# Optimization experiments

Measured on AMD Instinct MI355X. Metric: run time of the kernel, lower is better.

## Reference

```python
import jax, jax.numpy as jnp
import numpy as np

N_NODES = 100000
N_EDGES = 3200000
F_IN = 16
HID = 64
K = 4
N_LAYERS = 3
SLOPE = 0.01  # LeakyReLU default negative slope


def _gcn_norm(src, dst, edge_weight, n):
    # PyG gcn_norm with add_self_loops=False: deg over targets
    deg = jax.ops.segment_sum(edge_weight, dst, num_segments=n)
    dinv = jnp.where(deg > 0, jax.lax.rsqrt(jnp.maximum(deg, 1e-30)), 0.0)
    return dinv[src] * edge_weight * dinv[dst]


def _tag_conv(x, src, dst, norm, Ws, b):
    # out = sum_{k=0..K} (A_norm^k x) @ Ws[k] + b ; Ws: [K+1, in, out]
    out = x @ Ws[0]
    h = x
    for k in range(1, Ws.shape[0]):
        msg = norm[:, None] * h[src]                      # [E, in]
        h = jax.ops.segment_sum(msg, dst, num_segments=x.shape[0])
        out = out + h @ Ws[k]
    return out + b


def leaky_relu(x):
    return jnp.where(x >= 0, x, SLOPE * x)


def setup_inputs() -> dict:
    key = jax.random.key(0)
    ks = jax.random.split(key, 10)
    x = jax.random.normal(ks[0], (N_NODES, F_IN), dtype=jnp.float32)
    edge_index = jax.random.randint(ks[1], (2, N_EDGES), 0, N_NODES, dtype=jnp.int64)
    edge_weight = jax.random.uniform(ks[2], (N_EDGES,), dtype=jnp.float32)
    batch = jnp.zeros((N_NODES,), dtype=jnp.int64)
    s1 = 1.0 / np.sqrt(F_IN)
    s2 = 1.0 / np.sqrt(HID)
    W1 = jax.random.uniform(ks[3], (K + 1, F_IN, HID), jnp.float32, -s1, s1)
    b1 = jnp.zeros((HID,), jnp.float32)
    W2 = jax.random.uniform(ks[4], (N_LAYERS - 1, K + 1, HID, HID), jnp.float32, -s2, s2)
    b2 = jnp.zeros((N_LAYERS - 1, HID), jnp.float32)
    Wout = jax.random.uniform(ks[5], (HID, 1), jnp.float32, -s2, s2)
    bout = jnp.zeros((1,), jnp.float32)
    return {"x": x, "edge_index": edge_index, "edge_weight": edge_weight,
            "batch": batch, "W1": W1, "b1": b1, "W2": W2, "b2": b2,
            "Wout": Wout, "bout": bout}


def reference(x, edge_index, edge_weight, batch, W1, b1, W2, b2, Wout, bout):
    src, dst = edge_index[0], edge_index[1]
    norm = _gcn_norm(src, dst, edge_weight, x.shape[0])
    h = _tag_conv(x, src, dst, norm, W1, b1)
    h = leaky_relu(h)  # dropout p=0 -> identity (inference)
    for i in range(N_LAYERS - 1):
        h = _tag_conv(h, src, dst, norm, W2[i], b2[i])
        h = leaky_relu(h)
    # reghead_layers == 1 -> singleLinear
    return h @ Wout + bout
```

## Files before the change

kernel.cpp:

```cpp
#include <hip/hip_runtime.h>
#include <hip/hip_cooperative_groups.h>

namespace cg = cooperative_groups;


typedef unsigned long long u64;
typedef unsigned int u32;

__device__ __forceinline__ float h2f(unsigned short u) {
  _Float16 h;
  __builtin_memcpy(&h, &u, 2);
  return (float)h;
}
__device__ __forceinline__ unsigned short f2h(float f) {
  _Float16 h = (_Float16)f;
  unsigned short u;
  __builtin_memcpy(&u, &h, 2);
  return u;
}
__device__ __forceinline__ ushort4 pack_h(float4 v) {
  ushort4 r;
  r.x = f2h(v.x); r.y = f2h(v.y); r.z = f2h(v.z); r.w = f2h(v.w);
  return r;
}
__device__ __forceinline__ float4 unpack_h(ushort4 u) {
  return make_float4(h2f(u.x), h2f(u.y), h2f(u.z), h2f(u.w));
}
__device__ __forceinline__ void dec_ep(u32 u, int& s, float& w) {
  s = (int)(u & 0x1FFFFu);
  w = h2f((unsigned short)(u >> 17));
}


__global__ __launch_bounds__(256) void k_hist(const int* __restrict__ dst, u32* __restrict__ H,
                                              int E, int CH, int NB,
                                              const float4* __restrict__ x4,
                                              ushort4* __restrict__ xh, int n4) {
  __shared__ u32 hc[1024];
  int tid = threadIdx.x, blk = blockIdx.x, nblk = gridDim.x;
  for (int i = tid; i < 1024; i += 256) hc[i] = 0;
  for (int i = blk * 256 + tid; i < n4; i += nblk * 256) xh[i] = pack_h(x4[i]);
  __syncthreads();
  int e0 = blk * CH, e1 = min(E, e0 + CH);
  for (int e = e0 + tid; e < e1; e += 256) atomicAdd(&hc[((u32)dst[e]) >> 7], 1u);
  __syncthreads();
  for (int c = tid; c < NB; c += 256) H[(size_t)c * nblk + blk] = hc[c];
}

__global__ void scanH_blocks(u32* __restrict__ H, u32* __restrict__ bsum, int n) {
  __shared__ u32 s[256];
  int tid = threadIdx.x;
  int i = blockIdx.x * 256 + tid;
  u32 v = (i < n) ? H[i] : 0;
  s[tid] = v;
  __syncthreads();
#pragma unroll
  for (int off = 1; off < 256; off <<= 1) {
    u32 t = (tid >= off) ? s[tid - off] : 0;
    __syncthreads();
    s[tid] += t;
    __syncthreads();
  }
  if (i < n) H[i] = s[tid] - v;
  if (tid == 255) bsum[blockIdx.x] = s[255];
}

__global__ void scanH_sums(u32* __restrict__ bsum, int nb) {
  __shared__ u32 s[1024];
  int tid = threadIdx.x;
  u32 v = (tid < nb) ? bsum[tid] : 0;
  s[tid] = v;
  __syncthreads();
#pragma unroll
  for (int off = 1; off < 1024; off <<= 1) {
    u32 t = (tid >= off) ? s[tid - off] : 0;
    __syncthreads();
    s[tid] += t;
    __syncthreads();
  }
  if (tid < nb) bsum[tid] = s[tid] - v;
}

__global__ void scanH_add(u32* __restrict__ H, const u32* __restrict__ bsum, int n) {
  int i = blockIdx.x * blockDim.x + threadIdx.x;
  if (i < n) H[i] += bsum[i >> 8];
}

__global__ __launch_bounds__(256) void k_scatter(const int* __restrict__ src,
                                                 const int* __restrict__ dst,
                                                 const float* __restrict__ w,
                                                 const u32* __restrict__ H,
                                                 u64* __restrict__ sorted, int E, int CH, int NB) {
  __shared__ u32 cur[1024];
  int tid = threadIdx.x, blk = blockIdx.x, nblk = gridDim.x;
  for (int c = tid; c < NB; c += 256) cur[c] = H[(size_t)c * nblk + blk];
  __syncthreads();
  int e0 = blk * CH, e1 = min(E, e0 + CH);
  for (int e = e0 + tid; e < e1; e += 256) {
    int d = dst[e];
    int c = ((u32)d) >> 7;
    u32 p = atomicAdd(&cur[c], 1u);
    u64 it = (u64)(u32)src[e] | ((u64)((u32)d & 127u) << 17) |
             ((u64)__float_as_uint(w[e]) << 24);
    sorted[p] = it;
  }
}

#define BCAP 6144
__global__ __launch_bounds__(256) void k_bucket(u64* __restrict__ sorted,
                                                const u32* __restrict__ H, int NBLK,
                                                int* __restrict__ ptr, float* __restrict__ dinv,
                                                int N, int E, int NB) {
  __shared__ u64 stage[BCAP];
  __shared__ u32 cnt[128], base[128], cur[128], tmp[128];
  __shared__ float ws[128];
  int c = blockIdx.x, tid = threadIdx.x;
  int b0 = (int)H[(size_t)c * NBLK];
  int b1 = (c + 1 < NB) ? (int)H[(size_t)(c + 1) * NBLK] : E;
  int m = b1 - b0;
  if (tid < 128) { cnt[tid] = 0; ws[tid] = 0.f; }
  __syncthreads();
  for (int i = tid; i < m; i += 256) {
    u64 it = sorted[b0 + i];
    stage[i] = it;
    int lo = (int)((it >> 17) & 127u);
    atomicAdd(&cnt[lo], 1u);
    atomicAdd(&ws[lo], __uint_as_float((u32)(it >> 24)));
  }
  __syncthreads();
  u32 v = (tid < 128) ? cnt[tid] : 0;
  if (tid < 128) tmp[tid] = v;
  __syncthreads();
#pragma unroll
  for (int off = 1; off < 128; off <<= 1) {
    u32 t = 0;
    if (tid < 128 && tid >= off) t = tmp[tid - off];
    __syncthreads();
    if (tid < 128) tmp[tid] += t;
    __syncthreads();
  }
  if (tid < 128) {
    base[tid] = tmp[tid] - v;
    cur[tid] = tmp[tid] - v;
    int node = c * 128 + tid;
    if (node < N) {
      ptr[node] = b0 + (int)base[tid];
      float d = ws[tid];
      dinv[node] = (d > 0.f) ? rsqrtf(fmaxf(d, 1e-30f)) : 0.f;
    }
  }
  if (c == NB - 1 && tid == 0) ptr[N] = E;
  __syncthreads();
  for (int i = tid; i < m; i += 256) {
    u64 it = stage[i];
    int lo = (int)((it >> 17) & 127u);
    u32 p = atomicAdd(&cur[lo], 1u);
    sorted[b0 + (int)p] = it;
  }
}

__global__ __launch_bounds__(256) void k_pack(const u64* __restrict__ sorted,
                                              const float* __restrict__ dinv,
                                              const u32* __restrict__ H, int NBLK,
                                              u32* __restrict__ ep, int E, int NB) {
  int c = blockIdx.x;
  int b0 = (int)H[(size_t)c * NBLK];
  int b1 = (c + 1 < NB) ? (int)H[(size_t)(c + 1) * NBLK] : E;
  for (int i = b0 + threadIdx.x; i < b1; i += 256) {
    u64 it = sorted[i];
    int s = (int)(it & 0x1FFFFu);
    int dn = c * 128 + (int)((it >> 17) & 127u);
    float wv = __uint_as_float((u32)(it >> 24));
    float nv = dinv[s] * wv * dinv[dn];
    ep[i] = ((u32)f2h(nv) << 17) | (u32)s;
  }
}

__device__ __forceinline__ void acc_e(float4& a, u32 pe, ushort4 h) {
  float w = h2f((unsigned short)(pe >> 17));
  a.x = fmaf(w, h2f(h.x), a.x); a.y = fmaf(w, h2f(h.y), a.y);
  a.z = fmaf(w, h2f(h.z), a.z); a.w = fmaf(w, h2f(h.w), a.w);
}

template <int F4>
__device__ __forceinline__ float4 gather(const int* __restrict__ ptr, const u32* __restrict__ ep,
                                         const ushort4* __restrict__ hin, int node, int f4) {
  int e0 = ptr[node], e1 = ptr[node + 1];
  float4 a = make_float4(0.f, 0.f, 0.f, 0.f);
  int e = e0;
  while (e < e1 && (e & 3)) {
    u32 pe = ep[e];
    acc_e(a, pe, hin[(u32)(pe & 0x1FFFFu) * F4 + f4]);
    ++e;
  }
  int nq = (e1 - e) >> 2;
  if (nq > 0) {
    uint4 p = *(const uint4*)(ep + e);
    ushort4 h0 = hin[(u32)(p.x & 0x1FFFFu) * F4 + f4];
    ushort4 h1 = hin[(u32)(p.y & 0x1FFFFu) * F4 + f4];
    ushort4 h2 = hin[(u32)(p.z & 0x1FFFFu) * F4 + f4];
    ushort4 h3 = hin[(u32)(p.w & 0x1FFFFu) * F4 + f4];
    for (int q = 1; q < nq; ++q) {
      uint4 pn = *(const uint4*)(ep + e + 4 * q);
      ushort4 g0 = hin[(u32)(pn.x & 0x1FFFFu) * F4 + f4];
      ushort4 g1 = hin[(u32)(pn.y & 0x1FFFFu) * F4 + f4];
      ushort4 g2 = hin[(u32)(pn.z & 0x1FFFFu) * F4 + f4];
      ushort4 g3 = hin[(u32)(pn.w & 0x1FFFFu) * F4 + f4];
      acc_e(a, p.x, h0); acc_e(a, p.y, h1);
      acc_e(a, p.z, h2); acc_e(a, p.w, h3);
      p = pn; h0 = g0; h1 = g1; h2 = g2; h3 = g3;
    }
    acc_e(a, p.x, h0); acc_e(a, p.y, h1);
    acc_e(a, p.z, h2); acc_e(a, p.w, h3);
    e += nq * 4;
  }
  while (e < e1) {
    u32 pe = ep[e];
    acc_e(a, pe, hin[(u32)(pe & 0x1FFFFu) * F4 + f4]);
    ++e;
  }
  return a;
}

__device__ __forceinline__ void acc8(float4& a0, float4& a1, u32 pe, uint4 r) {
  float w = h2f((unsigned short)(pe >> 17));
  a0.x = fmaf(w, h2f((unsigned short)(r.x & 0xFFFFu)), a0.x);
  a0.y = fmaf(w, h2f((unsigned short)(r.x >> 16)), a0.y);
  a0.z = fmaf(w, h2f((unsigned short)(r.y & 0xFFFFu)), a0.z);
  a0.w = fmaf(w, h2f((unsigned short)(r.y >> 16)), a0.w);
  a1.x = fmaf(w, h2f((unsigned short)(r.z & 0xFFFFu)), a1.x);
  a1.y = fmaf(w, h2f((unsigned short)(r.z >> 16)), a1.y);
  a1.z = fmaf(w, h2f((unsigned short)(r.w & 0xFFFFu)), a1.z);
  a1.w = fmaf(w, h2f((unsigned short)(r.w >> 16)), a1.w);
}

__device__ __forceinline__ void gather64o(const int* __restrict__ ptr, const u32* __restrict__ ep,
                                          const ushort4* __restrict__ hin, int node,
                                          int f8, int o, float4& a0, float4& a1) {
  int e0 = ptr[node], e1 = ptr[node + 1];
  const u32 foff = 2u * (u32)f8;
  int e = e0;
  while (e < e1 && (e & 3)) {
    if ((e & 1) == o) {
      u32 pe = ep[e];
      uint4 r = *(const uint4*)(hin + ((u32)(pe & 0x1FFFFu) * 16u + foff));
      acc8(a0, a1, pe, r);
    }
    ++e;
  }
  int nq = (e1 - e) >> 2;
  int q = o;
  if (q < nq) {
    uint4 p = *(const uint4*)(ep + e + 4 * q);
    uint4 r0 = *(const uint4*)(hin + ((u32)(p.x & 0x1FFFFu) * 16u + foff));
    uint4 r1 = *(const uint4*)(hin + ((u32)(p.y & 0x1FFFFu) * 16u + foff));
    for (;;) {
      uint4 r2 = *(const uint4*)(hin + ((u32)(p.z & 0x1FFFFu) * 16u + foff));
      uint4 r3 = *(const uint4*)(hin + ((u32)(p.w & 0x1FFFFu) * 16u + foff));
      acc8(a0, a1, p.x, r0);
      acc8(a0, a1, p.y, r1);
      int qn = q + 2;
      if (qn >= nq) {
        acc8(a0, a1, p.z, r2);
        acc8(a0, a1, p.w, r3);
        break;
      }
      uint4 pn = *(const uint4*)(ep + e + 4 * qn);
      r0 = *(const uint4*)(hin + ((u32)(pn.x & 0x1FFFFu) * 16u + foff));
      r1 = *(const uint4*)(hin + ((u32)(pn.y & 0x1FFFFu) * 16u + foff));
      acc8(a0, a1, p.z, r2);
      acc8(a0, a1, p.w, r3);
      p = pn; q = qn;
    }
  }
  e += nq * 4;
  while (e < e1) {
    if ((e & 1) == o) {
      u32 pe = ep[e];
      uint4 r = *(const uint4*)(hin + ((u32)(pe & 0x1FFFFu) * 16u + foff));
      acc8(a0, a1, pe, r);
    }
    ++e;
  }
}

__device__ __forceinline__ void mm_acc(const float* __restrict__ tl, const float4* __restrict__ Wl,
                                       int ln, int j4, float4& a) {
#pragma unroll 8
  for (int i = 0; i < 64; ++i) {
    float tv = tl[ln * 64 + ((((i >> 2) ^ ln) << 2) | (i & 3))];
    float4 wv = Wl[i * 16 + j4];
    a.x = fmaf(tv, wv.x, a.x); a.y = fmaf(tv, wv.y, a.y);
    a.z = fmaf(tv, wv.z, a.z); a.w = fmaf(tv, wv.w, a.w);
  }
}

template <int NC>
__global__ __launch_bounds__(256) void mega_k(
    const int* __restrict__ ptr, const u32* __restrict__ ep,
    ushort4* __restrict__ hb0, ushort4* __restrict__ hb1, ushort4* __restrict__ hb2,
    const float* __restrict__ W2, const float* __restrict__ b2,
    const float* __restrict__ Wout, const float* __restrict__ bout,
    float* __restrict__ outv, int n) {
  cg::grid_group grid = cg::this_grid();
  __shared__ float4 Wl[1024];
  __shared__ float4 tl4[256];
  const float* tl = (const float*)tl4;
  const int tid = threadIdx.x, j4 = tid & 15, ln = tid >> 4;
  const int nb = (int)gridDim.x;
  float4 acc[NC];

  for (int L = 0; L < 2; ++L) {
    const float* WL = W2 + (size_t)L * 5 * 4096;
#pragma unroll
    for (int c = 0; c < NC; ++c) acc[c] = make_float4(0.f, 0.f, 0.f, 0.f);

    {
      const float4* W04 = (const float4*)WL;
      for (int i = tid; i < 1024; i += 256) Wl[i] = W04[i];
      __syncthreads();
#pragma unroll
      for (int c = 0; c < NC; ++c) {
        int node = (c * nb + (int)blockIdx.x) * 16 + ln;
        float4 own = make_float4(0.f, 0.f, 0.f, 0.f);
        if (node < n) own = unpack_h(hb2[(size_t)node * 16 + j4]);
        tl4[ln * 16 + (j4 ^ ln)] = own;
        mm_acc(tl, Wl, ln, j4, acc[c]);
      }
      __syncthreads();
    }

    for (int k = 1; k <= 4; ++k) {
      const ushort4* gsrc = (k == 1) ? hb2 : ((k == 3) ? hb1 : hb0);
      ushort4* gdst = (k == 2) ? hb1 : hb0;
      const bool last = (k == 4);
      const float4* Wk4 = (const float4*)(WL + (size_t)k * 4096);
      for (int i = tid; i < 1024; i += 256) Wl[i] = Wk4[i];
      __syncthreads();
#pragma unroll
      for (int c = 0; c < NC; ++c) {
        int node = (c * nb + (int)blockIdx.x) * 16 + ln;
        float4 t = make_float4(0.f, 0.f, 0.f, 0.f);
        if (node < n) {
          t = gather<16>(ptr, ep, gsrc, node, j4);
          if (!last) gdst[(size_t)node * 16 + j4] = pack_h(t);
        }
        tl4[ln * 16 + (j4 ^ ln)] = t;
        mm_acc(tl, Wl, ln, j4, acc[c]);
      }
      if (last) {
        const float4* bias4 = (const float4*)(b2 + (size_t)L * 64);
#pragma unroll
        for (int c = 0; c < NC; ++c) {
          int node = (c * nb + (int)blockIdx.x) * 16 + ln;
          if (node >= n) continue;
          float4 a = acc[c];
          float4 b = bias4[j4];
          a.x += b.x; a.y += b.y; a.z += b.z; a.w += b.w;
          a.x = (a.x >= 0.f) ? a.x : 0.01f * a.x;
          a.y = (a.y >= 0.f) ? a.y : 0.01f * a.y;
          a.z = (a.z >= 0.f) ? a.z : 0.01f * a.z;
          a.w = (a.w >= 0.f) ? a.w : 0.01f * a.w;
          if (L == 0) {
            hb2[(size_t)node * 16 + j4] = pack_h(a);
          } else {
            float v = a.x * Wout[4 * j4] + a.y * Wout[4 * j4 + 1] +
                      a.z * Wout[4 * j4 + 2] + a.w * Wout[4 * j4 + 3];
            v += __shfl_down(v, 8, 16);
            v += __shfl_down(v, 4, 16);
            v += __shfl_down(v, 2, 16);
            v += __shfl_down(v, 1, 16);
            if (j4 == 0) outv[node] = v + bout[0];
          }
        }
      }
      if (!(L == 1 && k == 4)) {
        __threadfence();
        grid.sync();
      }
    }
  }
}

template <bool FIRST, bool LAST, bool HEAD>
__launch_bounds__(256)
__global__ void ptag64_k(const int* __restrict__ ptr, const u32* __restrict__ ep,
                         const ushort4* __restrict__ hin, ushort4* __restrict__ hout,
                         const float4* __restrict__ Wk4, const float4* __restrict__ W04,
                         ushort4* __restrict__ acch, const float4* __restrict__ bias4,
                         const float* __restrict__ Wout, const float* __restrict__ bout,
                         float* __restrict__ outv, int n) {
  __shared__ float4 Wl[1024];
  __shared__ float4 tl4[256];
  const float* tl = (const float*)tl4;
  int tid = threadIdx.x;
  for (int i = tid; i < 1024; i += 256) Wl[i] = Wk4[i];
  int gid = blockIdx.x * 256 + tid;
  int node = gid >> 4, j4 = gid & 15, ln = tid >> 4;
  const int o = j4 >> 3, f8 = j4 & 7;

  float4 a0 = make_float4(0.f, 0.f, 0.f, 0.f);
  float4 a1 = make_float4(0.f, 0.f, 0.f, 0.f);
  if (node < n) gather64o(ptr, ep, hin, node, f8, o, a0, a1);
  a0.x += __shfl_xor(a0.x, 8, 16); a0.y += __shfl_xor(a0.y, 8, 16);
  a0.z += __shfl_xor(a0.z, 8, 16); a0.w += __shfl_xor(a0.w, 8, 16);
  a1.x += __shfl_xor(a1.x, 8, 16); a1.y += __shfl_xor(a1.y, 8, 16);
  a1.z += __shfl_xor(a1.z, 8, 16); a1.w += __shfl_xor(a1.w, 8, 16);
  float4 t = (o == 0) ? a0 : a1;
  int g = 2 * f8 + o;
  if (node < n && !LAST) hout[(size_t)node * 16 + g] = pack_h(t);
  tl4[ln * 16 + (g ^ ln)] = t;
  __syncthreads();

  float4 a = make_float4(0.f, 0.f, 0.f, 0.f);
  if (!FIRST && node < n) a = unpack_h(acch[(size_t)node * 16 + j4]);
  mm_acc(tl, Wl, ln, j4, a);
  if (FIRST) {
    __syncthreads();
    for (int i = tid; i < 1024; i += 256) Wl[i] = W04[i];
    float4 own = make_float4(0.f, 0.f, 0.f, 0.f);
    if (node < n) own = unpack_h(hin[(size_t)node * 16 + j4]);
    tl4[ln * 16 + (j4 ^ ln)] = own;
    __syncthreads();
    mm_acc(tl, Wl, ln, j4, a);
  }
  if (node >= n) return;

  if (LAST) {
    float4 b = bias4[j4];
    a.x += b.x; a.y += b.y; a.z += b.z; a.w += b.w;
    a.x = (a.x >= 0.f) ? a.x : 0.01f * a.x;
    a.y = (a.y >= 0.f) ? a.y : 0.01f * a.y;
    a.z = (a.z >= 0.f) ? a.z : 0.01f * a.z;
    a.w = (a.w >= 0.f) ? a.w : 0.01f * a.w;
    if (HEAD) {
      float v = a.x * Wout[4 * j4] + a.y * Wout[4 * j4 + 1] +
                a.z * Wout[4 * j4 + 2] + a.w * Wout[4 * j4 + 3];
      v += __shfl_down(v, 8, 16);
      v += __shfl_down(v, 4, 16);
      v += __shfl_down(v, 2, 16);
      v += __shfl_down(v, 1, 16);
      if (j4 == 0) outv[node] = v + bout[0];
    } else {
      hout[(size_t)node * 16 + j4] = pack_h(a);
    }
  } else {
    acch[(size_t)node * 16 + j4] = pack_h(a);
  }
}

template <bool FIRST, bool LAST>
__launch_bounds__(256)
__global__ void ptag16_k(const int* __restrict__ ptr, const u32* __restrict__ ep,
                         const ushort4* __restrict__ hin, ushort4* __restrict__ hout,
                         const float4* __restrict__ Wk4, const float4* __restrict__ W04,
                         ushort4* __restrict__ acch, const float4* __restrict__ bias4,
                         ushort4* __restrict__ outbuf, int n) {
  __shared__ float4 Wl[256];
  __shared__ float4 W0l[FIRST ? 256 : 1];
  __shared__ float4 tl4[64 * 5];
  const float* tl = (const float*)tl4;
  int tid = threadIdx.x;
  Wl[tid] = Wk4[tid];
  if (FIRST) W0l[tid] = W04[tid];
  int gid = blockIdx.x * 256 + tid;
  int node = gid >> 2, q = tid & 3, ln = tid >> 2;

  float4 t = make_float4(0.f, 0.f, 0.f, 0.f);
  if (node < n) {
    t = gather<4>(ptr, ep, hin, node, q);
    if (!LAST) hout[(size_t)node * 4 + q] = pack_h(t);
  }
  tl4[ln * 5 + q] = t;
  __syncthreads();

  float4 a[4];
#pragma unroll
  for (int c = 0; c < 4; ++c) a[c] = make_float4(0.f, 0.f, 0.f, 0.f);
  if (!FIRST && node < n) {
#pragma unroll
    for (int c = 0; c < 4; ++c) a[c] = unpack_h(acch[(size_t)node * 16 + 4 * q + c]);
  }
#pragma unroll 4
  for (int i = 0; i < 16; ++i) {
    float tv = tl[ln * 20 + i];
#pragma unroll
    for (int c = 0; c < 4; ++c) {
      float4 wv = Wl[i * 16 + 4 * q + c];
      a[c].x = fmaf(tv, wv.x, a[c].x); a[c].y = fmaf(tv, wv.y, a[c].y);
      a[c].z = fmaf(tv, wv.z, a[c].z); a[c].w = fmaf(tv, wv.w, a[c].w);
    }
  }
  if (FIRST) {
    __syncthreads();
    float4 own = make_float4(0.f, 0.f, 0.f, 0.f);
    if (node < n) own = unpack_h(hin[(size_t)node * 4 + q]);
    tl4[ln * 5 + q] = own;
    __syncthreads();
#pragma unroll 4
    for (int i = 0; i < 16; ++i) {
      float tv = tl[ln * 20 + i];
#pragma unroll
      for (int c = 0; c < 4; ++c) {
        float4 wv = W0l[i * 16 + 4 * q + c];
        a[c].x = fmaf(tv, wv.x, a[c].x); a[c].y = fmaf(tv, wv.y, a[c].y);
        a[c].z = fmaf(tv, wv.z, a[c].z); a[c].w = fmaf(tv, wv.w, a[c].w);
      }
    }
  }
  if (node >= n) return;

  if (LAST) {
#pragma unroll
    for (int c = 0; c < 4; ++c) {
      float4 b = bias4[4 * q + c];
      a[c].x += b.x; a[c].y += b.y; a[c].z += b.z; a[c].w += b.w;
      a[c].x = (a[c].x >= 0.f) ? a[c].x : 0.01f * a[c].x;
      a[c].y = (a[c].y >= 0.f) ? a[c].y : 0.01f * a[c].y;
      a[c].z = (a[c].z >= 0.f) ? a[c].z : 0.01f * a[c].z;
      a[c].w = (a[c].w >= 0.f) ? a[c].w : 0.01f * a[c].w;
      outbuf[(size_t)node * 16 + 4 * q + c] = pack_h(a[c]);
    }
  } else {
#pragma unroll
    for (int c = 0; c < 4; ++c) acch[(size_t)node * 16 + 4 * q + c] = pack_h(a[c]);
  }
}

extern "C" void kernel_launch(void* const* d_in, const int* in_sizes, int n_in,
                              void* d_out, int out_size, void* d_ws, size_t ws_size,
                              hipStream_t stream) {
  const float* x    = (const float*)d_in[0];
  const int*   ei   = (const int*)d_in[1];
  const float* ew   = (const float*)d_in[2];
  const float* W1   = (const float*)d_in[4];
  const float* b1   = (const float*)d_in[5];
  const float* W2   = (const float*)d_in[6];
  const float* b2   = (const float*)d_in[7];
  const float* Wout = (const float*)d_in[8];
  const float* bout = (const float*)d_in[9];
  float* out = (float*)d_out;

  const int N = in_sizes[0] / 16;
  const int E = in_sizes[2];
  const int* src = ei;
  const int* dst = ei + E;

  const int NBLK = 256;
  const int CH = (E + NBLK - 1) / NBLK;
  const int NB = (N + 127) >> 7;
  const int HN = NB * NBLK;

  char* ws = (char*)d_ws;
  size_t off = 0;
  auto alloc = [&](size_t bytes) {
    char* p = ws + off;
    off = (off + bytes + 255) & ~(size_t)255;
    return p;
  };
  u32*     H      = (u32*)alloc((size_t)HN * 4);
  u32*     bsum   = (u32*)alloc(4096);
  float*   dinv   = (float*)alloc((size_t)N * 4);
  int*     ptr    = (int*)alloc(((size_t)N + 1) * 4);
  u64*     sorted = (u64*)alloc((size_t)E * 8);
  u32*     ep     = (u32*)alloc((size_t)E * 4);
  ushort4* xh     = (ushort4*)alloc((size_t)N * 16 * 2);
  ushort4* hb0    = (ushort4*)alloc((size_t)N * 64 * 2);
  ushort4* hb1    = (ushort4*)alloc((size_t)N * 64 * 2);
  ushort4* hb2    = (ushort4*)alloc((size_t)N * 64 * 2);
  ushort4* acch   = (ushort4*)alloc((size_t)N * 64 * 2);

  k_hist<<<NBLK, 256, 0, stream>>>(dst, H, E, CH, NB, (const float4*)x, xh, N * 4);
  scanH_blocks<<<HN / 256, 256, 0, stream>>>(H, bsum, HN);
  scanH_sums<<<1, 1024, 0, stream>>>(bsum, HN / 256);
  scanH_add<<<HN / 256, 256, 0, stream>>>(H, bsum, HN);
  k_scatter<<<NBLK, 256, 0, stream>>>(src, dst, ew, H, sorted, E, CH, NB);
  k_bucket<<<NB, 256, 0, stream>>>(sorted, H, NBLK, ptr, dinv, N, E, NB);
  k_pack<<<NB, 256, 0, stream>>>(sorted, dinv, H, NBLK, ep, E, NB);

  int g4  = (N * 4 + 255) / 256;
  int g16 = (N * 16 + 255) / 256;

  auto W1k = [&](int k) { return (const float4*)(W1 + (size_t)k * 1024); };
  auto W2k = [&](int l, int k) { return (const float4*)(W2 + ((size_t)l * 5 + k) * 4096); };

  ptag16_k<true,  false><<<g4, 256, 0, stream>>>(ptr, ep, xh,  hb0, W1k(1), W1k(0), acch, nullptr, nullptr, N);
  ptag16_k<false, false><<<g4, 256, 0, stream>>>(ptr, ep, hb0, hb1, W1k(2), nullptr, acch, nullptr, nullptr, N);
  ptag16_k<false, false><<<g4, 256, 0, stream>>>(ptr, ep, hb1, hb0, W1k(3), nullptr, acch, nullptr, nullptr, N);
  ptag16_k<false, true ><<<g4, 256, 0, stream>>>(ptr, ep, hb0, nullptr, W1k(4), nullptr, acch,
                                                 (const float4*)b1, hb2, N);

  int maxB4 = 0, maxB5 = 0, maxB7 = 0;
  (void)hipOccupancyMaxActiveBlocksPerMultiprocessor(&maxB4, mega_k<4>, 256, 0);
  (void)hipOccupancyMaxActiveBlocksPerMultiprocessor(&maxB5, mega_k<5>, 256, 0);
  (void)hipOccupancyMaxActiveBlocksPerMultiprocessor(&maxB7, mega_k<7>, 256, 0);
  void* fn = nullptr;
  int grid = 0;
  if ((long)maxB4 * 256 * 16 * 4 >= (long)N) {
    fn = (void*)mega_k<4>; grid = maxB4 * 256;
  } else if ((long)maxB5 * 256 * 16 * 5 >= (long)N) {
    fn = (void*)mega_k<5>; grid = maxB5 * 256;
  } else if ((long)maxB7 * 256 * 16 * 7 >= (long)N) {
    fn = (void*)mega_k<7>; grid = maxB7 * 256;
  }

  if (fn) {
    const int* ptrA = ptr; const u32* epA = ep;
    ushort4 *h0A = hb0, *h1A = hb1, *h2A = hb2;
    const float *W2A = W2, *b2A = b2, *WoA = Wout, *boA = bout;
    float* outA = out; int nA = N;
    void* args[] = {&ptrA, &epA, &h0A, &h1A, &h2A, &W2A, &b2A, &WoA, &boA, &outA, &nA};
    hipLaunchCooperativeKernel(fn, dim3(grid), dim3(256), args, 0, stream);
  } else {
    ptag64_k<true,  false, false><<<g16, 256, 0, stream>>>(ptr, ep, hb2, hb0, W2k(0,1), W2k(0,0), acch,
                                                           nullptr, nullptr, nullptr, nullptr, N);
    ptag64_k<false, false, false><<<g16, 256, 0, stream>>>(ptr, ep, hb0, hb1, W2k(0,2), nullptr, acch,
                                                           nullptr, nullptr, nullptr, nullptr, N);
    ptag64_k<false, false, false><<<g16, 256, 0, stream>>>(ptr, ep, hb1, hb0, W2k(0,3), nullptr, acch,
                                                           nullptr, nullptr, nullptr, nullptr, N);
    ptag64_k<false, true,  false><<<g16, 256, 0, stream>>>(ptr, ep, hb0, hb2, W2k(0,4), nullptr, acch,
                                                           (const float4*)b2, nullptr, nullptr, nullptr, N);
    ptag64_k<true,  false, false><<<g16, 256, 0, stream>>>(ptr, ep, hb2, hb0, W2k(1,1), W2k(1,0), acch,
                                                           nullptr, nullptr, nullptr, nullptr, N);
    ptag64_k<false, false, false><<<g16, 256, 0, stream>>>(ptr, ep, hb0, hb1, W2k(1,2), nullptr, acch,
                                                           nullptr, nullptr, nullptr, nullptr, N);
    ptag64_k<false, false, false><<<g16, 256, 0, stream>>>(ptr, ep, hb1, hb0, W2k(1,3), nullptr, acch,
                                                           nullptr, nullptr, nullptr, nullptr, N);
    ptag64_k<false, true,  true ><<<g16, 256, 0, stream>>>(ptr, ep, hb0, nullptr, W2k(1,4), nullptr, acch,
                                                           (const float4*)(b2 + 64), Wout, bout, out, N);
  }
}
```

Baseline: 953.6 us.

## Drop cooperative mega-kernel; process four nodes per thread group in per-hop kernels

Removes the cooperative grid-synchronised mega kernel and always runs the per-hop 64-wide TAG kernels. Each 16-lane group now handles NC=4 nodes, so every weight element loaded from shared memory is reused across four node rows, and each weight tile is staged once per 64 nodes rather than once per 16. The intent is to cut grid.sync overhead and shared-memory weight traffic in exchange for more kernel launches, a larger LDS footprint (20KB+16KB) and more registers, which may lower occupancy for the latency-bound gather.

```diff
diff --git a/kernel.cpp b/kernel.cpp
--- a/kernel.cpp
+++ b/kernel.cpp
@@ -296,6 +296,22 @@
 }
 
 template <int NC>
+__device__ __forceinline__ void mm_acc_nc(const float* __restrict__ tl, const float4* __restrict__ Wl,
+                                          int ln, int j4, float4* acc) {
+#pragma unroll 8
+  for (int i = 0; i < 64; ++i) {
+    float4 wv = Wl[i * 16 + j4];
+    int sw = ln * 64 + ((((i >> 2) ^ ln) << 2) | (i & 3));
+#pragma unroll
+    for (int c = 0; c < NC; ++c) {
+      float tv = tl[c * 1024 + sw];
+      acc[c].x = fmaf(tv, wv.x, acc[c].x); acc[c].y = fmaf(tv, wv.y, acc[c].y);
+      acc[c].z = fmaf(tv, wv.z, acc[c].z); acc[c].w = fmaf(tv, wv.w, acc[c].w);
+    }
+  }
+}
+
+template <int NC>
 __global__ __launch_bounds__(256) void mega_k(
     const int* __restrict__ ptr, const u32* __restrict__ ep,
     ushort4* __restrict__ hb0, ushort4* __restrict__ hb1, ushort4* __restrict__ hb2,
@@ -314,7 +330,6 @@
     const float* WL = W2 + (size_t)L * 5 * 4096;
 #pragma unroll
     for (int c = 0; c < NC; ++c) acc[c] = make_float4(0.f, 0.f, 0.f, 0.f);
-
     {
       const float4* W04 = (const float4*)WL;
       for (int i = tid; i < 1024; i += 256) Wl[i] = W04[i];
@@ -329,7 +344,6 @@
       }
       __syncthreads();
     }
-
     for (int k = 1; k <= 4; ++k) {
       const ushort4* gsrc = (k == 1) ? hb2 : ((k == 3) ? hb1 : hb0);
       ushort4* gdst = (k == 2) ? hb1 : hb0;
@@ -382,70 +396,91 @@
   }
 }
 
-template <bool FIRST, bool LAST, bool HEAD>
+template <int NC, bool FIRST, bool LAST, bool HEAD>
 __launch_bounds__(256)
-__global__ void ptag64_k(const int* __restrict__ ptr, const u32* __restrict__ ep,
-                         const ushort4* __restrict__ hin, ushort4* __restrict__ hout,
-                         const float4* __restrict__ Wk4, const float4* __restrict__ W04,
-                         ushort4* __restrict__ acch, const float4* __restrict__ bias4,
-                         const float* __restrict__ Wout, const float* __restrict__ bout,
-                         float* __restrict__ outv, int n) {
+__global__ void ptag64nc_k(const int* __restrict__ ptr, const u32* __restrict__ ep,
+                           const ushort4* __restrict__ hin, ushort4* __restrict__ hout,
+                           const float4* __restrict__ Wk4, const float4* __restrict__ W04,
+                           ushort4* __restrict__ acch, const float4* __restrict__ bias4,
+                           const float* __restrict__ Wout, const float* __restrict__ bout,
+                           float* __restrict__ outv, int n) {
   __shared__ float4 Wl[1024];
-  __shared__ float4 tl4[256];
+  __shared__ float4 tl4[NC * 256];
   const float* tl = (const float*)tl4;
   int tid = threadIdx.x;
   for (int i = tid; i < 1024; i += 256) Wl[i] = Wk4[i];
-  int gid = blockIdx.x * 256 + tid;
-  int node = gid >> 4, j4 = gid & 15, ln = tid >> 4;
+  const int j4 = tid & 15, ln = tid >> 4;
   const int o = j4 >> 3, f8 = j4 & 7;
-
-  float4 a0 = make_float4(0.f, 0.f, 0.f, 0.f);
-  float4 a1 = make_float4(0.f, 0.f, 0.f, 0.f);
-  if (node < n) gather64o(ptr, ep, hin, node, f8, o, a0, a1);
-  a0.x += __shfl_xor(a0.x, 8, 16); a0.y += __shfl_xor(a0.y, 8, 16);
-  a0.z += __shfl_xor(a0.z, 8, 16); a0.w += __shfl_xor(a0.w, 8, 16);
-  a1.x += __shfl_xor(a1.x, 8, 16); a1.y += __shfl_xor(a1.y, 8, 16);
-  a1.z += __shfl_xor(a1.z, 8, 16); a1.w += __shfl_xor(a1.w, 8, 16);
-  float4 t = (o == 0) ? a0 : a1;
-  int g = 2 * f8 + o;
-  if (node < n && !LAST) hout[(size_t)node * 16 + g] = pack_h(t);
-  tl4[ln * 16 + (g ^ ln)] = t;
-  __syncthreads();
-
-  float4 a = make_float4(0.f, 0.f, 0.f, 0.f);
-  if (!FIRST && node < n) a = unpack_h(acch[(size_t)node * 16 + j4]);
-  mm_acc(tl, Wl, ln, j4, a);
+  const int nbase = (blockIdx.x * 16 + ln) * NC;
+
+#pragma unroll
+  for (int c = 0; c < NC; ++c) {
+    int node = nbase + c;
+    float4 a0 = make_float4(0.f, 0.f, 0.f, 0.f);
+    float4 a1 = make_float4(0.f, 0.f, 0.f, 0.f);
+    if (node < n) gather64o(ptr, ep, hin, node, f8, o, a0, a1);
+    a0.x += __shfl_xor(a0.x, 8, 16); a0.y += __shfl_xor(a0.y, 8, 16);
+    a0.z += __shfl_xor(a0.z, 8, 16); a0.w += __shfl_xor(a0.w, 8, 16);
+    a1.x += __shfl_xor(a1.x, 8, 16); a1.y += __shfl_xor(a1.y, 8, 16);
+    a1.z += __shfl_xor(a1.z, 8, 16); a1.w += __shfl_xor(a1.w, 8, 16);
+    float4 t = (o == 0) ? a0 : a1;
+    int g = 2 * f8 + o;
+    if (node < n && !LAST) hout[(size_t)node * 16 + g] = pack_h(t);
+    tl4[c * 256 + ln * 16 + (g ^ ln)] = t;
+  }
+  __syncthreads();
+
+  float4 acc[NC];
+#pragma unroll
+  for (int c = 0; c < NC; ++c) {
+    acc[c] = make_float4(0.f, 0.f, 0.f, 0.f);
+    if (!FIRST) {
+      int node = nbase + c;
+      if (node < n) acc[c] = unpack_h(acch[(size_t)node * 16 + j4]);
+    }
+  }
+  mm_acc_nc<NC>(tl, Wl, ln, j4, acc);
+
   if (FIRST) {
     __syncthreads();
     for (int i = tid; i < 1024; i += 256) Wl[i] = W04[i];
-    float4 own = make_float4(0.f, 0.f, 0.f, 0.f);
-    if (node < n) own = unpack_h(hin[(size_t)node * 16 + j4]);
-    tl4[ln * 16 + (j4 ^ ln)] = own;
-    __syncthreads();
-    mm_acc(tl, Wl, ln, j4, a);
-  }
-  if (node >= n) return;
-
-  if (LAST) {
-    float4 b = bias4[j4];
-    a.x += b.x; a.y += b.y; a.z += b.z; a.w += b.w;
-    a.x = (a.x >= 0.f) ? a.x : 0.01f * a.x;
-    a.y = (a.y >= 0.f) ? a.y : 0.01f * a.y;
-    a.z = (a.z >= 0.f) ? a.z : 0.01f * a.z;
-    a.w = (a.w >= 0.f) ? a.w : 0.01f * a.w;
-    if (HEAD) {
-      float v = a.x * Wout[4 * j4] + a.y * Wout[4 * j4 + 1] +
-                a.z * Wout[4 * j4 + 2] + a.w * Wout[4 * j4 + 3];
-      v += __shfl_down(v, 8, 16);
-      v += __shfl_down(v, 4, 16);
-      v += __shfl_down(v, 2, 16);
-      v += __shfl_down(v, 1, 16);
-      if (j4 == 0) outv[node] = v + bout[0];
+#pragma unroll
+    for (int c = 0; c < NC; ++c) {
+      int node = nbase + c;
+      float4 own = make_float4(0.f, 0.f, 0.f, 0.f);
+      if (node < n) own = unpack_h(hin[(size_t)node * 16 + j4]);
+      tl4[c * 256 + ln * 16 + (j4 ^ ln)] = own;
+    }
+    __syncthreads();
+    mm_acc_nc<NC>(tl, Wl, ln, j4, acc);
+  }
+
+#pragma unroll
+  for (int c = 0; c < NC; ++c) {
+    int node = nbase + c;
+    if (node >= n) continue;
+    float4 a = acc[c];
+    if (LAST) {
+      float4 b = bias4[j4];
+      a.x += b.x; a.y += b.y; a.z += b.z; a.w += b.w;
+      a.x = (a.x >= 0.f) ? a.x : 0.01f * a.x;
+      a.y = (a.y >= 0.f) ? a.y : 0.01f * a.y;
+      a.z = (a.z >= 0.f) ? a.z : 0.01f * a.z;
+      a.w = (a.w >= 0.f) ? a.w : 0.01f * a.w;
+      if (HEAD) {
+        float v = a.x * Wout[4 * j4] + a.y * Wout[4 * j4 + 1] +
+                  a.z * Wout[4 * j4 + 2] + a.w * Wout[4 * j4 + 3];
+        v += __shfl_down(v, 8, 16);
+        v += __shfl_down(v, 4, 16);
+        v += __shfl_down(v, 2, 16);
+        v += __shfl_down(v, 1, 16);
+        if (j4 == 0) outv[node] = v + bout[0];
+      } else {
+        hout[(size_t)node * 16 + j4] = pack_h(a);
+      }
     } else {
-      hout[(size_t)node * 16 + j4] = pack_h(a);
-    }
-  } else {
-    acch[(size_t)node * 16 + j4] = pack_h(a);
+      acch[(size_t)node * 16 + j4] = pack_h(a);
+    }
   }
 }
 
@@ -578,8 +613,9 @@
   k_bucket<<<NB, 256, 0, stream>>>(sorted, H, NBLK, ptr, dinv, N, E, NB);
   k_pack<<<NB, 256, 0, stream>>>(sorted, dinv, H, NBLK, ep, E, NB);
 
-  int g4  = (N * 4 + 255) / 256;
-  int g16 = (N * 16 + 255) / 256;
+  int g4 = (N * 4 + 255) / 256;
+  constexpr int NCP = 4;
+  int g64 = (N + 16 * NCP - 1) / (16 * NCP);
 
   auto W1k = [&](int k) { return (const float4*)(W1 + (size_t)k * 1024); };
   auto W2k = [&](int l, int k) { return (const float4*)(W2 + ((size_t)l * 5 + k) * 4096); };
@@ -590,43 +626,20 @@
   ptag16_k<false, true ><<<g4, 256, 0, stream>>>(ptr, ep, hb0, nullptr, W1k(4), nullptr, acch,
                                                  (const float4*)b1, hb2, N);
 
-  int maxB4 = 0, maxB5 = 0, maxB7 = 0;
-  (void)hipOccupancyMaxActiveBlocksPerMultiprocessor(&maxB4, mega_k<4>, 256, 0);
-  (void)hipOccupancyMaxActiveBlocksPerMultiprocessor(&maxB5, mega_k<5>, 256, 0);
-  (void)hipOccupancyMaxActiveBlocksPerMultiprocessor(&maxB7, mega_k<7>, 256, 0);
-  void* fn = nullptr;
-  int grid = 0;
-  if ((long)maxB4 * 256 * 16 * 4 >= (long)N) {
-    fn = (void*)mega_k<4>; grid = maxB4 * 256;
-  } else if ((long)maxB5 * 256 * 16 * 5 >= (long)N) {
-    fn = (void*)mega_k<5>; grid = maxB5 * 256;
-  } else if ((long)maxB7 * 256 * 16 * 7 >= (long)N) {
-    fn = (void*)mega_k<7>; grid = maxB7 * 256;
-  }
-
-  if (fn) {
-    const int* ptrA = ptr; const u32* epA = ep;
-    ushort4 *h0A = hb0, *h1A = hb1, *h2A = hb2;
-    const float *W2A = W2, *b2A = b2, *WoA = Wout, *boA = bout;
-    float* outA = out; int nA = N;
-    void* args[] = {&ptrA, &epA, &h0A, &h1A, &h2A, &W2A, &b2A, &WoA, &boA, &outA, &nA};
-    hipLaunchCooperativeKernel(fn, dim3(grid), dim3(256), args, 0, stream);
-  } else {
-    ptag64_k<true,  false, false><<<g16, 256, 0, stream>>>(ptr, ep, hb2, hb0, W2k(0,1), W2k(0,0), acch,
-                                                           nullptr, nullptr, nullptr, nullptr, N);
-    ptag64_k<false, false, false><<<g16, 256, 0, stream>>>(ptr, ep, hb0, hb1, W2k(0,2), nullptr, acch,
-                                                           nullptr, nullptr, nullptr, nullptr, N);
-    ptag64_k<false, false, false><<<g16, 256, 0, stream>>>(ptr, ep, hb1, hb0, W2k(0,3), nullptr, acch,
-                                                           nullptr, nullptr, nullptr, nullptr, N);
-    ptag64_k<false, true,  false><<<g16, 256, 0, stream>>>(ptr, ep, hb0, hb2, W2k(0,4), nullptr, acch,
-                                                           (const float4*)b2, nullptr, nullptr, nullptr, N);
-    ptag64_k<true,  false, false><<<g16, 256, 0, stream>>>(ptr, ep, hb2, hb0, W2k(1,1), W2k(1,0), acch,
-                                                           nullptr, nullptr, nullptr, nullptr, N);
-    ptag64_k<false, false, false><<<g16, 256, 0, stream>>>(ptr, ep, hb0, hb1, W2k(1,2), nullptr, acch,
-                                                           nullptr, nullptr, nullptr, nullptr, N);
-    ptag64_k<false, false, false><<<g16, 256, 0, stream>>>(ptr, ep, hb1, hb0, W2k(1,3), nullptr, acch,
-                                                           nullptr, nullptr, nullptr, nullptr, N);
-    ptag64_k<false, true,  true ><<<g16, 256, 0, stream>>>(ptr, ep, hb0, nullptr, W2k(1,4), nullptr, acch,
-                                                           (const float4*)(b2 + 64), Wout, bout, out, N);
-  }
-}
+  ptag64nc_k<NCP, true,  false, false><<<g64, 256, 0, stream>>>(ptr, ep, hb2, hb0, W2k(0,1), W2k(0,0), acch,
+                                                                nullptr, nullptr, nullptr, nullptr, N);
+  ptag64nc_k<NCP, false, false, false><<<g64, 256, 0, stream>>>(ptr, ep, hb0, hb1, W2k(0,2), nullptr, acch,
+                                                                nullptr, nullptr, nullptr, nullptr, N);
+  ptag64nc_k<NCP, false, false, false><<<g64, 256, 0, stream>>>(ptr, ep, hb1, hb0, W2k(0,3), nullptr, acch,
+                                                                nullptr, nullptr, nullptr, nullptr, N);
+  ptag64nc_k<NCP, false, true,  false><<<g64, 256, 0, stream>>>(ptr, ep, hb0, hb2, W2k(0,4), nullptr, acch,
+                                                                (const float4*)b2, nullptr, nullptr, nullptr, N);
+  ptag64nc_k<NCP, true,  false, false><<<g64, 256, 0, stream>>>(ptr, ep, hb2, hb0, W2k(1,1), W2k(1,0), acch,
+                                                                nullptr, nullptr, nullptr, nullptr, N);
+  ptag64nc_k<NCP, false, false, false><<<g64, 256, 0, stream>>>(ptr, ep, hb0, hb1, W2k(1,2), nullptr, acch,
+                                                                nullptr, nullptr, nullptr, nullptr, N);
+  ptag64nc_k<NCP, false, false, false><<<g64, 256, 0, stream>>>(ptr, ep, hb1, hb0, W2k(1,3), nullptr, acch,
+                                                                nullptr, nullptr, nullptr, nullptr, N);
+  ptag64nc_k<NCP, false, true,  true ><<<g64, 256, 0, stream>>>(ptr, ep, hb0, nullptr, W2k(1,4), nullptr, acch,
+                                                                (const float4*)(b2 + 64), Wout, bout, out, N);
+}
```

New measurement: 1.111 ms. 1.16x slower.

## Replace cooperative megakernel with degree-sorted node permutation across per-hop kernels

Applied to the files above, without the earlier changes.

Builds a per-node degree histogram, scans it, and scatters nodes into a permutation grouped by in-degree. Every gather/matmul kernel then processes nodes through this permutation, so nodes with similar edge counts share a wavefront and divergence is reduced. The cooperative grid-synced megakernel for the 64-wide layers is removed in favour of always launching separate per-hop kernels. This adds five small preprocessing launches and an indirection load per node, and gives up the locality of contiguous node ordering for the writes to the hidden buffers.

```diff
diff --git a/kernel.cpp b/kernel.cpp
--- a/kernel.cpp
+++ b/kernel.cpp
@@ -1,7 +1,4 @@
 #include <hip/hip_runtime.h>
-#include <hip/hip_cooperative_groups.h>
-
-namespace cg = cooperative_groups;
 
 
 typedef unsigned long long u64;
@@ -173,6 +170,39 @@
     float wv = __uint_as_float((u32)(it >> 24));
     float nv = dinv[s] * wv * dinv[dn];
     ep[i] = ((u32)f2h(nv) << 17) | (u32)s;
+  }
+}
+
+
+__global__ __launch_bounds__(256) void k_dhist(const int* __restrict__ ptr, u32* __restrict__ DH,
+                                               int N, int CHN) {
+  __shared__ u32 h[256];
+  int tid = threadIdx.x, blk = blockIdx.x;
+  h[tid] = 0;
+  __syncthreads();
+  int i0 = blk * CHN, i1 = min(N, i0 + CHN);
+  for (int i = i0 + tid; i < i1; i += 256) {
+    int d = ptr[i + 1] - ptr[i];
+    if (d > 255) d = 255;
+    atomicAdd(&h[d], 1u);
+  }
+  __syncthreads();
+  DH[(size_t)tid * 256 + blk] = h[tid];
+}
+
+__global__ __launch_bounds__(256) void k_dscatter(const int* __restrict__ ptr,
+                                                  const u32* __restrict__ DH,
+                                                  int* __restrict__ perm, int N, int CHN) {
+  __shared__ u32 cur[256];
+  int tid = threadIdx.x, blk = blockIdx.x;
+  cur[tid] = DH[(size_t)tid * 256 + blk];
+  __syncthreads();
+  int i0 = blk * CHN, i1 = min(N, i0 + CHN);
+  for (int i = i0 + tid; i < i1; i += 256) {
+    int d = ptr[i + 1] - ptr[i];
+    if (d > 255) d = 255;
+    u32 p = atomicAdd(&cur[d], 1u);
+    perm[p] = i;
   }
 }
 
@@ -295,96 +325,10 @@
   }
 }
 
-template <int NC>
-__global__ __launch_bounds__(256) void mega_k(
-    const int* __restrict__ ptr, const u32* __restrict__ ep,
-    ushort4* __restrict__ hb0, ushort4* __restrict__ hb1, ushort4* __restrict__ hb2,
-    const float* __restrict__ W2, const float* __restrict__ b2,
-    const float* __restrict__ Wout, const float* __restrict__ bout,
-    float* __restrict__ outv, int n) {
-  cg::grid_group grid = cg::this_grid();
-  __shared__ float4 Wl[1024];
-  __shared__ float4 tl4[256];
-  const float* tl = (const float*)tl4;
-  const int tid = threadIdx.x, j4 = tid & 15, ln = tid >> 4;
-  const int nb = (int)gridDim.x;
-  float4 acc[NC];
-
-  for (int L = 0; L < 2; ++L) {
-    const float* WL = W2 + (size_t)L * 5 * 4096;
-#pragma unroll
-    for (int c = 0; c < NC; ++c) acc[c] = make_float4(0.f, 0.f, 0.f, 0.f);
-
-    {
-      const float4* W04 = (const float4*)WL;
-      for (int i = tid; i < 1024; i += 256) Wl[i] = W04[i];
-      __syncthreads();
-#pragma unroll
-      for (int c = 0; c < NC; ++c) {
-        int node = (c * nb + (int)blockIdx.x) * 16 + ln;
-        float4 own = make_float4(0.f, 0.f, 0.f, 0.f);
-        if (node < n) own = unpack_h(hb2[(size_t)node * 16 + j4]);
-        tl4[ln * 16 + (j4 ^ ln)] = own;
-        mm_acc(tl, Wl, ln, j4, acc[c]);
-      }
-      __syncthreads();
-    }
-
-    for (int k = 1; k <= 4; ++k) {
-      const ushort4* gsrc = (k == 1) ? hb2 : ((k == 3) ? hb1 : hb0);
-      ushort4* gdst = (k == 2) ? hb1 : hb0;
-      const bool last = (k == 4);
-      const float4* Wk4 = (const float4*)(WL + (size_t)k * 4096);
-      for (int i = tid; i < 1024; i += 256) Wl[i] = Wk4[i];
-      __syncthreads();
-#pragma unroll
-      for (int c = 0; c < NC; ++c) {
-        int node = (c * nb + (int)blockIdx.x) * 16 + ln;
-        float4 t = make_float4(0.f, 0.f, 0.f, 0.f);
-        if (node < n) {
-          t = gather<16>(ptr, ep, gsrc, node, j4);
-          if (!last) gdst[(size_t)node * 16 + j4] = pack_h(t);
-        }
-        tl4[ln * 16 + (j4 ^ ln)] = t;
-        mm_acc(tl, Wl, ln, j4, acc[c]);
-      }
-      if (last) {
-        const float4* bias4 = (const float4*)(b2 + (size_t)L * 64);
-#pragma unroll
-        for (int c = 0; c < NC; ++c) {
-          int node = (c * nb + (int)blockIdx.x) * 16 + ln;
-          if (node >= n) continue;
-          float4 a = acc[c];
-          float4 b = bias4[j4];
-          a.x += b.x; a.y += b.y; a.z += b.z; a.w += b.w;
-          a.x = (a.x >= 0.f) ? a.x : 0.01f * a.x;
-          a.y = (a.y >= 0.f) ? a.y : 0.01f * a.y;
-          a.z = (a.z >= 0.f) ? a.z : 0.01f * a.z;
-          a.w = (a.w >= 0.f) ? a.w : 0.01f * a.w;
-          if (L == 0) {
-            hb2[(size_t)node * 16 + j4] = pack_h(a);
-          } else {
-            float v = a.x * Wout[4 * j4] + a.y * Wout[4 * j4 + 1] +
-                      a.z * Wout[4 * j4 + 2] + a.w * Wout[4 * j4 + 3];
-            v += __shfl_down(v, 8, 16);
-            v += __shfl_down(v, 4, 16);
-            v += __shfl_down(v, 2, 16);
-            v += __shfl_down(v, 1, 16);
-            if (j4 == 0) outv[node] = v + bout[0];
-          }
-        }
-      }
-      if (!(L == 1 && k == 4)) {
-        __threadfence();
-        grid.sync();
-      }
-    }
-  }
-}
-
 template <bool FIRST, bool LAST, bool HEAD>
 __launch_bounds__(256)
 __global__ void ptag64_k(const int* __restrict__ ptr, const u32* __restrict__ ep,
+                         const int* __restrict__ perm,
                          const ushort4* __restrict__ hin, ushort4* __restrict__ hout,
                          const float4* __restrict__ Wk4, const float4* __restrict__ W04,
                          ushort4* __restrict__ acch, const float4* __restrict__ bias4,
@@ -395,8 +339,9 @@
   const float* tl = (const float*)tl4;
   int tid = threadIdx.x;
   for (int i = tid; i < 1024; i += 256) Wl[i] = Wk4[i];
-  int gid = blockIdx.x * 256 + tid;
-  int node = gid >> 4, j4 = gid & 15, ln = tid >> 4;
+  int j4 = tid & 15, ln = tid >> 4;
+  int slot = blockIdx.x * 16 + ln;
+  int node = (slot < n) ? perm[slot] : n;
   const int o = j4 >> 3, f8 = j4 & 7;
 
   float4 a0 = make_float4(0.f, 0.f, 0.f, 0.f);
@@ -452,6 +397,7 @@
 template <bool FIRST, bool LAST>
 __launch_bounds__(256)
 __global__ void ptag16_k(const int* __restrict__ ptr, const u32* __restrict__ ep,
+                         const int* __restrict__ perm,
                          const ushort4* __restrict__ hin, ushort4* __restrict__ hout,
                          const float4* __restrict__ Wk4, const float4* __restrict__ W04,
                          ushort4* __restrict__ acch, const float4* __restrict__ bias4,
@@ -464,7 +410,8 @@
   Wl[tid] = Wk4[tid];
   if (FIRST) W0l[tid] = W04[tid];
   int gid = blockIdx.x * 256 + tid;
-  int node = gid >> 2, q = tid & 3, ln = tid >> 2;
+  int slot = gid >> 2, q = tid & 3, ln = tid >> 2;
+  int node = (slot < n) ? perm[slot] : n;
 
   float4 t = make_float4(0.f, 0.f, 0.f, 0.f);
   if (node < n) {
@@ -550,6 +497,7 @@
   const int CH = (E + NBLK - 1) / NBLK;
   const int NB = (N + 127) >> 7;
   const int HN = NB * NBLK;
+  const int CHN = (N + NBLK - 1) / NBLK;
 
   char* ws = (char*)d_ws;
   size_t off = 0;
@@ -564,6 +512,8 @@
   int*     ptr    = (int*)alloc(((size_t)N + 1) * 4);
   u64*     sorted = (u64*)alloc((size_t)E * 8);
   u32*     ep     = (u32*)alloc((size_t)E * 4);
+  u32*     DH     = (u32*)alloc((size_t)256 * 256 * 4);
+  int*     perm   = (int*)alloc((size_t)N * 4);
   ushort4* xh     = (ushort4*)alloc((size_t)N * 16 * 2);
   ushort4* hb0    = (ushort4*)alloc((size_t)N * 64 * 2);
   ushort4* hb1    = (ushort4*)alloc((size_t)N * 64 * 2);
@@ -578,55 +528,38 @@
   k_bucket<<<NB, 256, 0, stream>>>(sorted, H, NBLK, ptr, dinv, N, E, NB);
   k_pack<<<NB, 256, 0, stream>>>(sorted, dinv, H, NBLK, ep, E, NB);
 
+  k_dhist<<<256, 256, 0, stream>>>(ptr, DH, N, CHN);
+  scanH_blocks<<<256, 256, 0, stream>>>(DH, bsum, 65536);
+  scanH_sums<<<1, 1024, 0, stream>>>(bsum, 256);
+  scanH_add<<<256, 256, 0, stream>>>(DH, bsum, 65536);
+  k_dscatter<<<256, 256, 0, stream>>>(ptr, DH, perm, N, CHN);
+
   int g4  = (N * 4 + 255) / 256;
   int g16 = (N * 16 + 255) / 256;
 
   auto W1k = [&](int k) { return (const float4*)(W1 + (size_t)k * 1024); };
   auto W2k = [&](int l, int k) { return (const float4*)(W2 + ((size_t)l * 5 + k) * 4096); };
 
-  ptag16_k<true,  false><<<g4, 256, 0, stream>>>(ptr, ep, xh,  hb0, W1k(1), W1k(0), acch, nullptr, nullptr, N);
-  ptag16_k<false, false><<<g4, 256, 0, stream>>>(ptr, ep, hb0, hb1, W1k(2), nullptr, acch, nullptr, nullptr, N);
-  ptag16_k<false, false><<<g4, 256, 0, stream>>>(ptr, ep, hb1, hb0, W1k(3), nullptr, acch, nullptr, nullptr, N);
-  ptag16_k<false, true ><<<g4, 256, 0, stream>>>(ptr, ep, hb0, nullptr, W1k(4), nullptr, acch,
+  ptag16_k<true,  false><<<g4, 256, 0, stream>>>(ptr, ep, perm, xh,  hb0, W1k(1), W1k(0), acch, nullptr, nullptr, N);
+  ptag16_k<false, false><<<g4, 256, 0, stream>>>(ptr, ep, perm, hb0, hb1, W1k(2), nullptr, acch, nullptr, nullptr, N);
+  ptag16_k<false, false><<<g4, 256, 0, stream>>>(ptr, ep, perm, hb1, hb0, W1k(3), nullptr, acch, nullptr, nullptr, N);
+  ptag16_k<false, true ><<<g4, 256, 0, stream>>>(ptr, ep, perm, hb0, nullptr, W1k(4), nullptr, acch,
                                                  (const float4*)b1, hb2, N);
 
-  int maxB4 = 0, maxB5 = 0, maxB7 = 0;
-  (void)hipOccupancyMaxActiveBlocksPerMultiprocessor(&maxB4, mega_k<4>, 256, 0);
-  (void)hipOccupancyMaxActiveBlocksPerMultiprocessor(&maxB5, mega_k<5>, 256, 0);
-  (void)hipOccupancyMaxActiveBlocksPerMultiprocessor(&maxB7, mega_k<7>, 256, 0);
-  void* fn = nullptr;
-  int grid = 0;
-  if ((long)maxB4 * 256 * 16 * 4 >= (long)N) {
-    fn = (void*)mega_k<4>; grid = maxB4 * 256;
-  } else if ((long)maxB5 * 256 * 16 * 5 >= (long)N) {
-    fn = (void*)mega_k<5>; grid = maxB5 * 256;
-  } else if ((long)maxB7 * 256 * 16 * 7 >= (long)N) {
-    fn = (void*)mega_k<7>; grid = maxB7 * 256;
-  }
-
-  if (fn) {
-    const int* ptrA = ptr; const u32* epA = ep;
-    ushort4 *h0A = hb0, *h1A = hb1, *h2A = hb2;
-    const float *W2A = W2, *b2A = b2, *WoA = Wout, *boA = bout;
-    float* outA = out; int nA = N;
-    void* args[] = {&ptrA, &epA, &h0A, &h1A, &h2A, &W2A, &b2A, &WoA, &boA, &outA, &nA};
-    hipLaunchCooperativeKernel(fn, dim3(grid), dim3(256), args, 0, stream);
-  } else {
-    ptag64_k<true,  false, false><<<g16, 256, 0, stream>>>(ptr, ep, hb2, hb0, W2k(0,1), W2k(0,0), acch,
-                                                           nullptr, nullptr, nullptr, nullptr, N);
-    ptag64_k<false, false, false><<<g16, 256, 0, stream>>>(ptr, ep, hb0, hb1, W2k(0,2), nullptr, acch,
-                                                           nullptr, nullptr, nullptr, nullptr, N);
-    ptag64_k<false, false, false><<<g16, 256, 0, stream>>>(ptr, ep, hb1, hb0, W2k(0,3), nullptr, acch,
-                                                           nullptr, nullptr, nullptr, nullptr, N);
-    ptag64_k<false, true,  false><<<g16, 256, 0, stream>>>(ptr, ep, hb0, hb2, W2k(0,4), nullptr, acch,
-                                                           (const float4*)b2, nullptr, nullptr, nullptr, N);
-    ptag64_k<true,  false, false><<<g16, 256, 0, stream>>>(ptr, ep, hb2, hb0, W2k(1,1), W2k(1,0), acch,
-                                                           nullptr, nullptr, nullptr, nullptr, N);
-    ptag64_k<false, false, false><<<g16, 256, 0, stream>>>(ptr, ep, hb0, hb1, W2k(1,2), nullptr, acch,
-                                                           nullptr, nullptr, nullptr, nullptr, N);
-    ptag64_k<false, false, false><<<g16, 256, 0, stream>>>(ptr, ep, hb1, hb0, W2k(1,3), nullptr, acch,
-                                                           nullptr, nullptr, nullptr, nullptr, N);
-    ptag64_k<false, true,  true ><<<g16, 256, 0, stream>>>(ptr, ep, hb0, nullptr, W2k(1,4), nullptr, acch,
-                                                           (const float4*)(b2 + 64), Wout, bout, out, N);
-  }
-}
+  ptag64_k<true,  false, false><<<g16, 256, 0, stream>>>(ptr, ep, perm, hb2, hb0, W2k(0,1), W2k(0,0), acch,
+                                                         nullptr, nullptr, nullptr, nullptr, N);
+  ptag64_k<false, false, false><<<g16, 256, 0, stream>>>(ptr, ep, perm, hb0, hb1, W2k(0,2), nullptr, acch,
+                                                         nullptr, nullptr, nullptr, nullptr, N);
+  ptag64_k<false, false, false><<<g16, 256, 0, stream>>>(ptr, ep, perm, hb1, hb0, W2k(0,3), nullptr, acch,
+                                                         nullptr, nullptr, nullptr, nullptr, N);
+  ptag64_k<false, true,  false><<<g16, 256, 0, stream>>>(ptr, ep, perm, hb0, hb2, W2k(0,4), nullptr, acch,
+                                                         (const float4*)b2, nullptr, nullptr, nullptr, N);
+  ptag64_k<true,  false, false><<<g16, 256, 0, stream>>>(ptr, ep, perm, hb2, hb0, W2k(1,1), W2k(1,0), acch,
+                                                         nullptr, nullptr, nullptr, nullptr, N);
+  ptag64_k<false, false, false><<<g16, 256, 0, stream>>>(ptr, ep, perm, hb0, hb1, W2k(1,2), nullptr, acch,
+                                                         nullptr, nullptr, nullptr, nullptr, N);
+  ptag64_k<false, false, false><<<g16, 256, 0, stream>>>(ptr, ep, perm, hb1, hb0, W2k(1,3), nullptr, acch,
+                                                         nullptr, nullptr, nullptr, nullptr, N);
+  ptag64_k<false, true,  true ><<<g16, 256, 0, stream>>>(ptr, ep, perm, hb0, nullptr, W2k(1,4), nullptr, acch,
+                                                         (const float4*)(b2 + 64), Wout, bout, out, N);
+}
```

Result: slower. 973.7 us (+2.1%).
